# Kernel tuning notes

Hardware: AMD Instinct MI355X
Metric: run time of the kernel (lower is better)

## Reference

```python
import jax, jax.numpy as jnp
import numpy as np

B, S, D = 8, 4096, 1024


def setup_inputs() -> dict:
    key = jax.random.key(0)
    kq, kk, kv, kw, kb = jax.random.split(key, 5)
    query = jax.random.normal(kq, (B, S, D), dtype=jnp.float32)
    k = jax.random.normal(kk, (B, S, D), dtype=jnp.float32)
    value = jax.random.normal(kv, (B, S, D), dtype=jnp.float32)
    # nn.Linear(hidden_size, hidden_size) params (Kaiming-uniform-ish init scale)
    bound = 1.0 / np.sqrt(D)
    W_out = jax.random.uniform(kw, (D, D), minval=-bound, maxval=bound, dtype=jnp.float32)
    b_out = jax.random.uniform(kb, (D,), minval=-bound, maxval=bound, dtype=jnp.float32)
    return {"query": query, "key": k, "value": value, "W_out": W_out, "b_out": b_out}


def reference(query, key, value, W_out, b_out):
    d = query.shape[-1]
    scale = 1.0 / jnp.sqrt(jnp.asarray(d, dtype=query.dtype))
    # scores: [B, Sq, Sk]
    scores = jnp.einsum("bqd,bkd->bqk", query, key) * scale
    attn = jax.nn.softmax(scores, axis=-1)
    # training=False -> dropout is identity
    ctx = jnp.einsum("bqk,bkd->bqd", attn, value)
    # nn.Linear: x @ W^T + b
    out = jnp.einsum("bqd,ed->bqe", ctx, W_out) + b_out
    return out
```

## Files before the change

kernel.cpp:

```cpp
#include <hip/hip_runtime.h>
#include <hip/hip_bf16.h>

typedef __attribute__((ext_vector_type(4))) float f4;
typedef __attribute__((ext_vector_type(4))) short s4;
typedef __attribute__((ext_vector_type(8))) short s8;

#define SEQ 4096
#define DIM 1024
#define NB 8

__device__ inline short f2bf(float f) {
    return __builtin_bit_cast(short, __float2bfloat16(f));
}

__device__ inline float bf2f(short s) {
    return __builtin_bit_cast(float, (unsigned)((unsigned short)s) << 16);
}

__device__ inline void gload_lds16(const void* g, void* l) {
    __builtin_amdgcn_global_load_lds(
        (const __attribute__((address_space(1))) void*)g,
        (__attribute__((address_space(3))) void*)l, 16, 0, 0);
}

template<int OUT>
__global__ __launch_bounds__(512, 2) void gemm256(
    const short* __restrict__ A, size_t lda, size_t bsA,
    const short* __restrict__ B, size_t ldb, size_t bsB,
    void* __restrict__ C, size_t ldc, size_t bsC,
    const float* __restrict__ bias, int nt, int gridN)
{
    __shared__ short lds[2 * 32768];
    const int tid  = threadIdx.x;
    const int lane = tid & 63;
    const int wave = tid >> 6;

    A += (size_t)blockIdx.y * bsA;
    B += (size_t)blockIdx.y * bsB;
    float* Cf = (float*)C + (size_t)blockIdx.y * bsC;
    short* Cs = (short*)C + (size_t)blockIdx.y * bsC;

    const int nwg = gridDim.x;
    int wg = blockIdx.x;
    wg = (wg & 7) * (nwg >> 3) + (wg >> 3);
    const size_t tm = (size_t)(wg / gridN) * 256;
    const size_t tn = (size_t)(wg % gridN) * 256;

    const int srow = tid >> 3;
    const int slot = tid & 7;
    const int sc   = slot ^ (srow & 7);
    const short* pA = A + (tm + srow) * lda + sc * 8;
    const short* pB = B + (tn + srow) * ldb + sc * 8;
    const int ldst = srow * 64 + slot * 8;

    const int fr = lane & 15, kg = lane >> 4;
    const int wr = wave >> 2, wc = wave & 3;

    auto STAGE = [&](int t) {
        short* bufA = lds + (t & 1) * 32768;
        short* bufB = bufA + 16384;
        const size_t k0 = (size_t)t * 64;
        #pragma unroll
        for (int j = 0; j < 4; ++j) {
            gload_lds16(pA + (size_t)(j * 64) * lda + k0, bufA + j * 4096 + ldst);
            gload_lds16(pB + (size_t)(j * 64) * ldb + k0, bufB + j * 4096 + ldst);
        }
    };

    f4 acc[8][4];
    #pragma unroll
    for (int m = 0; m < 8; ++m)
        #pragma unroll
        for (int n = 0; n < 4; ++n)
            acc[m][n] = (f4){0.f, 0.f, 0.f, 0.f};

    STAGE(0);
    __syncthreads();

    for (int t = 0; t < nt; ++t) {
        if (t + 1 < nt) STAGE(t + 1);

        const short* bufA = lds + (t & 1) * 32768;
        const short* bufB = bufA + 16384;
        s8 af[2][8], bf[2][4];
        #pragma unroll
        for (int kh = 0; kh < 2; ++kh) {
            #pragma unroll
            for (int m = 0; m < 8; ++m) {
                const int row = wr * 128 + m * 16 + fr;
                const int c   = kh * 4 + kg;
                af[kh][m] = *(const s8*)(bufA + row * 64 + (c ^ (row & 7)) * 8);
            }
            #pragma unroll
            for (int n = 0; n < 4; ++n) {
                const int row = wc * 64 + n * 16 + fr;
                const int c   = kh * 4 + kg;
                bf[kh][n] = *(const s8*)(bufB + row * 64 + (c ^ (row & 7)) * 8);
            }
        }
        __builtin_amdgcn_s_setprio(1);
        #pragma unroll
        for (int kh = 0; kh < 2; ++kh)
            #pragma unroll
            for (int m = 0; m < 8; ++m)
                #pragma unroll
                for (int n = 0; n < 4; ++n)
                    acc[m][n] = __builtin_amdgcn_mfma_f32_16x16x32_bf16(
                        af[kh][m], bf[kh][n], acc[m][n], 0, 0, 0);
        __builtin_amdgcn_s_setprio(0);

        __syncthreads();
    }

    const int cg = lane >> 4, cl = lane & 15;
    #pragma unroll
    for (int m = 0; m < 8; ++m) {
        #pragma unroll
        for (int n = 0; n < 4; ++n) {
            const size_t grow = tm + wr * 128 + m * 16 + cg * 4;
            const size_t gcol = tn + wc * 64 + n * 16 + cl;
            float bv = 0.f;
            if constexpr (OUT == 0) { if (bias) bv = bias[gcol]; }
            #pragma unroll
            for (int i = 0; i < 4; ++i) {
                const float val = acc[m][n][i] + bv;
                if constexpr (OUT == 0)
                    Cf[(grow + i) * ldc + gcol] = val;
                else
                    Cs[(grow + i) * ldc + gcol] = f2bf(val);
            }
        }
    }
}

__global__ __launch_bounds__(256) void conv_bf16(const float* __restrict__ in,
                                                 short* __restrict__ out, int n8)
{
    const int i = blockIdx.x * 256 + threadIdx.x;
    if (i >= n8) return;
    f4 a = ((const f4*)in)[2 * i];
    f4 b = ((const f4*)in)[2 * i + 1];
    s8 w;
    w[0] = f2bf(a[0]); w[1] = f2bf(a[1]); w[2] = f2bf(a[2]); w[3] = f2bf(a[3]);
    w[4] = f2bf(b[0]); w[5] = f2bf(b[1]); w[6] = f2bf(b[2]); w[7] = f2bf(b[3]);
    ((s8*)out)[i] = w;
}

__global__ __launch_bounds__(256) void prep_batch(
    const float* __restrict__ Qf, const float* __restrict__ Kf,
    const float* __restrict__ Vf,
    short* __restrict__ Qb, short* __restrict__ Kb, short* __restrict__ VT)
{
    const int tid = threadIdx.x;
    const int blk = blockIdx.x;

    if (blk < 4096) {
        const float* in = (blk < 2048) ? Qf : Kf;
        short* out      = (blk < 2048) ? Qb : Kb;
        const int i = (blk & 2047) * 256 + tid;
        f4 a = ((const f4*)in)[2 * i];
        f4 b = ((const f4*)in)[2 * i + 1];
        s8 w;
        w[0] = f2bf(a[0]); w[1] = f2bf(a[1]); w[2] = f2bf(a[2]); w[3] = f2bf(a[3]);
        w[4] = f2bf(b[0]); w[5] = f2bf(b[1]); w[6] = f2bf(b[2]); w[7] = f2bf(b[3]);
        ((s8*)out)[i] = w;
    } else {
        __shared__ float t[32][33];
        const int b2 = blk - 4096;
        const size_t k0 = (size_t)(b2 & 127) * 32;
        const size_t d0 = (size_t)(b2 >> 7) * 32;

        const int r = tid >> 3, c4 = (tid & 7) * 4;
        f4 x = *(const f4*)(Vf + (k0 + r) * DIM + d0 + c4);
        #pragma unroll
        for (int i = 0; i < 4; ++i) t[r][c4 + i] = x[i];
        __syncthreads();

        const int d = tid >> 3, kk = (tid & 7) * 4;
        s4 w;
        #pragma unroll
        for (int i = 0; i < 4; ++i) w[i] = f2bf(t[kk + i][d]);
        *(s4*)(VT + (d0 + d) * SEQ + k0 + kk) = w;
    }
}

__global__ __launch_bounds__(256) void softmax_rows_bf(short* __restrict__ scores)
{
    const int tid = threadIdx.x;
    short* srow = scores + (size_t)blockIdx.y * SEQ * SEQ + (size_t)blockIdx.x * SEQ;
    const float SCALE = 0.03125f;

    float v[16];
    float mx = -3.4e38f;
    #pragma unroll
    for (int j = 0; j < 4; ++j) {
        s4 h = *(const s4*)(srow + (size_t)(j * 256 + tid) * 4);
        #pragma unroll
        for (int i = 0; i < 4; ++i) {
            const float f = bf2f(h[i]) * SCALE;
            v[j * 4 + i] = f;
            mx = fmaxf(mx, f);
        }
    }
    #pragma unroll
    for (int o = 32; o > 0; o >>= 1) mx = fmaxf(mx, __shfl_xor(mx, o));
    __shared__ float red[4];
    if ((tid & 63) == 0) red[tid >> 6] = mx;
    __syncthreads();
    mx = fmaxf(fmaxf(red[0], red[1]), fmaxf(red[2], red[3]));

    float sum = 0.f;
    #pragma unroll
    for (int j = 0; j < 16; ++j) {
        const float e = __expf(v[j] - mx);
        v[j] = e;
        sum += e;
    }
    #pragma unroll
    for (int o = 32; o > 0; o >>= 1) sum += __shfl_xor(sum, o);
    __syncthreads();
    if ((tid & 63) == 0) red[tid >> 6] = sum;
    __syncthreads();
    const float inv = 1.f / (red[0] + red[1] + red[2] + red[3]);

    #pragma unroll
    for (int j = 0; j < 4; ++j) {
        s4 w;
        #pragma unroll
        for (int i = 0; i < 4; ++i) w[i] = f2bf(v[j * 4 + i] * inv);
        *(s4*)(srow + (size_t)(j * 256 + tid) * 4) = w;
    }
}

extern "C" void kernel_launch(void* const* d_in, const int* in_sizes, int n_in,
                              void* d_out, int out_size, void* d_ws, size_t ws_size,
                              hipStream_t stream) {
    const float* Q    = (const float*)d_in[0];
    const float* Km   = (const float*)d_in[1];
    const float* V    = (const float*)d_in[2];
    const float* W    = (const float*)d_in[3];
    const float* bias = (const float*)d_in[4];
    float* out = (float*)d_out;

    short* ctx = (short*)d_ws;
    short* VT4 = ctx + (size_t)NB * SEQ * DIM;
    short* Qb  = VT4 + (size_t)4 * DIM * SEQ;
    short* Kb  = Qb + (size_t)SEQ * DIM;
    short* Wb  = Kb + (size_t)SEQ * DIM;
    short* scoresB = (short*)d_out;

    const dim3 blk256(256), blk512(512);
    conv_bf16<<<DIM * DIM / 2048, blk256, 0, stream>>>(W, Wb, DIM * DIM / 8);

    for (int g = 0; g < 2; ++g) {
        for (int b4 = 0; b4 < 4; ++b4) {
            const int b = g * 4 + b4;
            const float* Qf = Q  + (size_t)b * SEQ * DIM;
            const float* Kf = Km + (size_t)b * SEQ * DIM;
            const float* Vf = V  + (size_t)b * SEQ * DIM;

            prep_batch<<<dim3(8192), blk256, 0, stream>>>(
                Qf, Kf, Vf, Qb, Kb, VT4 + (size_t)b4 * DIM * SEQ);

            gemm256<2><<<dim3(256, 1), blk512, 0, stream>>>(
                Qb, DIM, 0, Kb, DIM, 0,
                scoresB + (size_t)b4 * SEQ * SEQ, SEQ, 0,
                nullptr, DIM / 64, 16);
        }
        softmax_rows_bf<<<dim3(SEQ, 4), blk256, 0, stream>>>(scoresB);

        gemm256<2><<<dim3(64, 4), blk512, 0, stream>>>(
            scoresB, SEQ, (size_t)SEQ * SEQ,
            VT4, SEQ, (size_t)DIM * SEQ,
            ctx + (size_t)g * 4 * SEQ * DIM, DIM, (size_t)SEQ * DIM,
            nullptr, SEQ / 64, 4);
    }

    gemm256<0><<<dim3(512, 1), blk512, 0, stream>>>(
        ctx, DIM, 0, Wb, DIM, 0, out, DIM, 0, bias, DIM / 64, 4);
}
```

Baseline: 811.8 us.

## Split GEMM LDS staging into half-tiles with explicit vmcnt-based prefetch pipeline

Restructures the 256x256 bf16 GEMM main loop so that LDS holds four half-tile buffers instead of two full-tile buffers. Loads for the next two half-tiles are issued right after the fragment reads finish, so they overlap with the MFMA block. Synchronisation moves from __syncthreads to explicit vmcnt/lgkmcnt waits plus raw s_barrier, which removes the full drain of outstanding loads each iteration. The risk is subtle: the hand-counted vmcnt thresholds and buffer reuse must match the number of loads in flight, or races appear.

```diff
diff --git a/kernel.cpp b/kernel.cpp
--- a/kernel.cpp
+++ b/kernel.cpp
@@ -30,7 +30,7 @@
     void* __restrict__ C, size_t ldc, size_t bsC,
     const float* __restrict__ bias, int nt, int gridN)
 {
-    __shared__ short lds[2 * 32768];
+    __shared__ short lds[4 * 16384];
     const int tid  = threadIdx.x;
     const int lane = tid & 63;
     const int wave = tid >> 6;
@@ -56,14 +56,14 @@
     const int fr = lane & 15, kg = lane >> 4;
     const int wr = wave >> 2, wc = wave & 3;
 
-    auto STAGE = [&](int t) {
-        short* bufA = lds + (t & 1) * 32768;
-        short* bufB = bufA + 16384;
-        const size_t k0 = (size_t)t * 64;
-        #pragma unroll
-        for (int j = 0; j < 4; ++j) {
-            gload_lds16(pA + (size_t)(j * 64) * lda + k0, bufA + j * 4096 + ldst);
-            gload_lds16(pB + (size_t)(j * 64) * ldb + k0, bufB + j * 4096 + ldst);
+    auto SH = [&](int h) {
+        short* hb = lds + (h & 3) * 16384;
+        const size_t k0 = (size_t)(h >> 1) * 64;
+        const size_t rb = (size_t)(h & 1) * 128;
+        #pragma unroll
+        for (int j = 0; j < 2; ++j) {
+            gload_lds16(pA + (rb + j * 64) * lda + k0, hb + j * 4096 + ldst);
+            gload_lds16(pB + (rb + j * 64) * ldb + k0, hb + 8192 + j * 4096 + ldst);
         }
     };
 
@@ -74,30 +74,38 @@
         for (int n = 0; n < 4; ++n)
             acc[m][n] = (f4){0.f, 0.f, 0.f, 0.f};
 
-    STAGE(0);
-    __syncthreads();
+    SH(0); SH(1); SH(2); SH(3);
+    asm volatile("s_waitcnt vmcnt(8)" ::: "memory");
+    __builtin_amdgcn_s_barrier();
+    __builtin_amdgcn_sched_barrier(0);
 
     for (int t = 0; t < nt; ++t) {
-        if (t + 1 < nt) STAGE(t + 1);
-
-        const short* bufA = lds + (t & 1) * 32768;
-        const short* bufB = bufA + 16384;
+        const short* hb0 = lds + ((2 * t) & 3) * 16384;
+        const short* hb1 = lds + ((2 * t + 1) & 3) * 16384;
+        const short* hA = wr ? hb1 : hb0;
+        const short* hB = ((wc >> 1) ? hb1 : hb0) + 8192;
+
         s8 af[2][8], bf[2][4];
         #pragma unroll
         for (int kh = 0; kh < 2; ++kh) {
             #pragma unroll
             for (int m = 0; m < 8; ++m) {
-                const int row = wr * 128 + m * 16 + fr;
-                const int c   = kh * 4 + kg;
-                af[kh][m] = *(const s8*)(bufA + row * 64 + (c ^ (row & 7)) * 8);
+                const int rh = m * 16 + fr;
+                af[kh][m] = *(const s8*)(hA + rh * 64 + ((kh * 4 + kg) ^ (rh & 7)) * 8);
             }
             #pragma unroll
             for (int n = 0; n < 4; ++n) {
-                const int row = wc * 64 + n * 16 + fr;
-                const int c   = kh * 4 + kg;
-                bf[kh][n] = *(const s8*)(bufB + row * 64 + (c ^ (row & 7)) * 8);
-            }
-        }
+                const int rh = (wc & 1) * 64 + n * 16 + fr;
+                bf[kh][n] = *(const s8*)(hB + rh * 64 + ((kh * 4 + kg) ^ (rh & 7)) * 8);
+            }
+        }
+        asm volatile("s_waitcnt lgkmcnt(0)" ::: "memory");
+        __builtin_amdgcn_sched_barrier(0);
+        __builtin_amdgcn_s_barrier();
+        __builtin_amdgcn_sched_barrier(0);
+
+        if (t + 2 < nt) { SH(2 * t + 4); SH(2 * t + 5); }
+
         __builtin_amdgcn_s_setprio(1);
         #pragma unroll
         for (int kh = 0; kh < 2; ++kh)
@@ -109,7 +117,15 @@
                         af[kh][m], bf[kh][n], acc[m][n], 0, 0, 0);
         __builtin_amdgcn_s_setprio(0);
 
-        __syncthreads();
+        if (t + 1 < nt) {
+            if (t + 2 < nt) {
+                asm volatile("s_waitcnt vmcnt(8)" ::: "memory");
+            } else {
+                asm volatile("s_waitcnt vmcnt(0)" ::: "memory");
+            }
+            __builtin_amdgcn_s_barrier();
+            __builtin_amdgcn_sched_barrier(0);
+        }
     }
 
     const int cg = lane >> 4, cl = lane & 15;
```

Result: slower. 829.6 us (+2.2%).

## Shrink GEMM tile to 128x256 with BK=32 for four blocks per CU

Applied to the files above, without the earlier changes.

Replaces the 256x256x64 GEMM tile with a 128x256x32 tile, new swizzled LDS staging, and launch bounds requesting four 512-thread blocks per CU. LDS use drops to 48KB and the accumulators to a 4x4 MFMA set, so more waves can be resident to hide latency, and grids double so there are more blocks to spread across CUs. In exchange each tile has lower arithmetic intensity (more global and LDS traffic per FLOP) and runs twice as many K iterations, each with a barrier.

```diff
diff --git a/kernel.cpp b/kernel.cpp
--- a/kernel.cpp
+++ b/kernel.cpp
@@ -24,13 +24,13 @@
 }
 
 template<int OUT>
-__global__ __launch_bounds__(512, 2) void gemm256(
+__global__ __launch_bounds__(512, 4) void gemmB(
     const short* __restrict__ A, size_t lda, size_t bsA,
     const short* __restrict__ B, size_t ldb, size_t bsB,
     void* __restrict__ C, size_t ldc, size_t bsC,
     const float* __restrict__ bias, int nt, int gridN)
 {
-    __shared__ short lds[2 * 32768];
+    __shared__ short lds[2 * 12288];
     const int tid  = threadIdx.x;
     const int lane = tid & 63;
     const int wave = tid >> 6;
@@ -43,33 +43,30 @@
     const int nwg = gridDim.x;
     int wg = blockIdx.x;
     wg = (wg & 7) * (nwg >> 3) + (wg >> 3);
-    const size_t tm = (size_t)(wg / gridN) * 256;
+    const size_t tm = (size_t)(wg / gridN) * 128;
     const size_t tn = (size_t)(wg % gridN) * 256;
 
-    const int srow = tid >> 3;
-    const int slot = tid & 7;
-    const int sc   = slot ^ (srow & 7);
+    const int srow = tid >> 2;
+    const int sc   = (tid & 3) ^ ((tid >> 3) & 3);
     const short* pA = A + (tm + srow) * lda + sc * 8;
     const short* pB = B + (tn + srow) * ldb + sc * 8;
-    const int ldst = srow * 64 + slot * 8;
+    const size_t b128 = (size_t)128 * ldb;
 
     const int fr = lane & 15, kg = lane >> 4;
+    const int ck = kg ^ ((fr >> 1) & 3);
     const int wr = wave >> 2, wc = wave & 3;
 
     auto STAGE = [&](int t) {
-        short* bufA = lds + (t & 1) * 32768;
-        short* bufB = bufA + 16384;
-        const size_t k0 = (size_t)t * 64;
-        #pragma unroll
-        for (int j = 0; j < 4; ++j) {
-            gload_lds16(pA + (size_t)(j * 64) * lda + k0, bufA + j * 4096 + ldst);
-            gload_lds16(pB + (size_t)(j * 64) * ldb + k0, bufB + j * 4096 + ldst);
-        }
+        short* buf = lds + (t & 1) * 12288;
+        const size_t k0 = (size_t)t * 32;
+        gload_lds16(pA + k0,        buf + tid * 8);
+        gload_lds16(pB + k0,        buf + 4096 + tid * 8);
+        gload_lds16(pB + b128 + k0, buf + 8192 + tid * 8);
     };
 
-    f4 acc[8][4];
-    #pragma unroll
-    for (int m = 0; m < 8; ++m)
+    f4 acc[4][4];
+    #pragma unroll
+    for (int m = 0; m < 4; ++m)
         #pragma unroll
         for (int n = 0; n < 4; ++n)
             acc[m][n] = (f4){0.f, 0.f, 0.f, 0.f};
@@ -80,33 +77,26 @@
     for (int t = 0; t < nt; ++t) {
         if (t + 1 < nt) STAGE(t + 1);
 
-        const short* bufA = lds + (t & 1) * 32768;
-        const short* bufB = bufA + 16384;
-        s8 af[2][8], bf[2][4];
-        #pragma unroll
-        for (int kh = 0; kh < 2; ++kh) {
+        const short* bufA = lds + (t & 1) * 12288;
+        const short* bufB = bufA + 4096;
+        s8 af[4], bf[4];
+        #pragma unroll
+        for (int m = 0; m < 4; ++m) {
+            const int row = wr * 64 + m * 16 + fr;
+            af[m] = *(const s8*)(bufA + row * 32 + ck * 8);
+        }
+        #pragma unroll
+        for (int n = 0; n < 4; ++n) {
+            const int row = wc * 64 + n * 16 + fr;
+            bf[n] = *(const s8*)(bufB + row * 32 + ck * 8);
+        }
+        __builtin_amdgcn_s_setprio(1);
+        #pragma unroll
+        for (int m = 0; m < 4; ++m)
             #pragma unroll
-            for (int m = 0; m < 8; ++m) {
-                const int row = wr * 128 + m * 16 + fr;
-                const int c   = kh * 4 + kg;
-                af[kh][m] = *(const s8*)(bufA + row * 64 + (c ^ (row & 7)) * 8);
-            }
-            #pragma unroll
-            for (int n = 0; n < 4; ++n) {
-                const int row = wc * 64 + n * 16 + fr;
-                const int c   = kh * 4 + kg;
-                bf[kh][n] = *(const s8*)(bufB + row * 64 + (c ^ (row & 7)) * 8);
-            }
-        }
-        __builtin_amdgcn_s_setprio(1);
-        #pragma unroll
-        for (int kh = 0; kh < 2; ++kh)
-            #pragma unroll
-            for (int m = 0; m < 8; ++m)
-                #pragma unroll
-                for (int n = 0; n < 4; ++n)
-                    acc[m][n] = __builtin_amdgcn_mfma_f32_16x16x32_bf16(
-                        af[kh][m], bf[kh][n], acc[m][n], 0, 0, 0);
+            for (int n = 0; n < 4; ++n)
+                acc[m][n] = __builtin_amdgcn_mfma_f32_16x16x32_bf16(
+                    af[m], bf[n], acc[m][n], 0, 0, 0);
         __builtin_amdgcn_s_setprio(0);
 
         __syncthreads();
@@ -114,10 +104,10 @@
 
     const int cg = lane >> 4, cl = lane & 15;
     #pragma unroll
-    for (int m = 0; m < 8; ++m) {
+    for (int m = 0; m < 4; ++m) {
         #pragma unroll
         for (int n = 0; n < 4; ++n) {
-            const size_t grow = tm + wr * 128 + m * 16 + cg * 4;
+            const size_t grow = tm + wr * 64 + m * 16 + cg * 4;
             const size_t gcol = tn + wc * 64 + n * 16 + cl;
             float bv = 0.f;
             if constexpr (OUT == 0) { if (bias) bv = bias[gcol]; }
@@ -262,20 +252,20 @@
             prep_batch<<<dim3(8192), blk256, 0, stream>>>(
                 Qf, Kf, Vf, Qb, Kb, VT4 + (size_t)b4 * DIM * SEQ);
 
-            gemm256<2><<<dim3(256, 1), blk512, 0, stream>>>(
+            gemmB<2><<<dim3(512, 1), blk512, 0, stream>>>(
                 Qb, DIM, 0, Kb, DIM, 0,
                 scoresB + (size_t)b4 * SEQ * SEQ, SEQ, 0,
-                nullptr, DIM / 64, 16);
+                nullptr, DIM / 32, 16);
         }
         softmax_rows_bf<<<dim3(SEQ, 4), blk256, 0, stream>>>(scoresB);
 
-        gemm256<2><<<dim3(64, 4), blk512, 0, stream>>>(
+        gemmB<2><<<dim3(128, 4), blk512, 0, stream>>>(
             scoresB, SEQ, (size_t)SEQ * SEQ,
             VT4, SEQ, (size_t)DIM * SEQ,
             ctx + (size_t)g * 4 * SEQ * DIM, DIM, (size_t)SEQ * DIM,
-            nullptr, SEQ / 64, 4);
-    }
-
-    gemm256<0><<<dim3(512, 1), blk512, 0, stream>>>(
-        ctx, DIM, 0, Wb, DIM, 0, out, DIM, 0, bias, DIM / 64, 4);
-}
+            nullptr, SEQ / 32, 4);
+    }
+
+    gemmB<0><<<dim3(1024, 1), blk512, 0, stream>>>(
+        ctx, DIM, 0, Wb, DIM, 0, out, DIM, 0, bias, DIM / 32, 4);
+}
```

New measurement: 872.3 us. +7.4%, slower.

## Split GEMM main loop into four phases interleaving LDS reads, prefetch, and MFMA

Applied to the files above, without the earlier changes.

Restructures the bf16 GEMM main loop into four sub-phases per K-tile. Each phase loads a slice of A fragments from LDS, issues one quarter of the next tile's global-to-LDS prefetch, and runs the matching MFMAs, with explicit barriers and waitcnts in place of one bulk load and a single __syncthreads. The aim is to overlap memory traffic with matrix work and cut register pressure from holding all A fragments at once. The extra per-phase barriers add synchronisation cost and could stall waves.

```diff
diff --git a/kernel.cpp b/kernel.cpp
--- a/kernel.cpp
+++ b/kernel.cpp
@@ -56,15 +56,12 @@
     const int fr = lane & 15, kg = lane >> 4;
     const int wr = wave >> 2, wc = wave & 3;
 
-    auto STAGE = [&](int t) {
+    auto STAGE2 = [&](int t, int p) {
         short* bufA = lds + (t & 1) * 32768;
         short* bufB = bufA + 16384;
         const size_t k0 = (size_t)t * 64;
-        #pragma unroll
-        for (int j = 0; j < 4; ++j) {
-            gload_lds16(pA + (size_t)(j * 64) * lda + k0, bufA + j * 4096 + ldst);
-            gload_lds16(pB + (size_t)(j * 64) * ldb + k0, bufB + j * 4096 + ldst);
-        }
+        gload_lds16(pA + (size_t)(p * 64) * lda + k0, bufA + p * 4096 + ldst);
+        gload_lds16(pB + (size_t)(p * 64) * ldb + k0, bufB + p * 4096 + ldst);
     };
 
     f4 acc[8][4];
@@ -74,42 +71,56 @@
         for (int n = 0; n < 4; ++n)
             acc[m][n] = (f4){0.f, 0.f, 0.f, 0.f};
 
-    STAGE(0);
+    STAGE2(0, 0); STAGE2(0, 1); STAGE2(0, 2); STAGE2(0, 3);
     __syncthreads();
 
     for (int t = 0; t < nt; ++t) {
-        if (t + 1 < nt) STAGE(t + 1);
-
         const short* bufA = lds + (t & 1) * 32768;
         const short* bufB = bufA + 16384;
-        s8 af[2][8], bf[2][4];
-        #pragma unroll
-        for (int kh = 0; kh < 2; ++kh) {
+        s8 bfrag[2][4];
+
+        #pragma unroll
+        for (int p = 0; p < 4; ++p) {
+            if (p == 0) {
+                #pragma unroll
+                for (int kh = 0; kh < 2; ++kh)
+                    #pragma unroll
+                    for (int n = 0; n < 4; ++n) {
+                        const int row = wc * 64 + n * 16 + fr;
+                        bfrag[kh][n] = *(const s8*)(bufB + row * 64 + (((kh * 4 + kg) ^ (row & 7)) * 8));
+                    }
+            }
+            s8 afrag[2][2];
             #pragma unroll
-            for (int m = 0; m < 8; ++m) {
-                const int row = wr * 128 + m * 16 + fr;
-                const int c   = kh * 4 + kg;
-                af[kh][m] = *(const s8*)(bufA + row * 64 + (c ^ (row & 7)) * 8);
-            }
+            for (int kh = 0; kh < 2; ++kh)
+                #pragma unroll
+                for (int m2 = 0; m2 < 2; ++m2) {
+                    const int row = wr * 128 + (2 * p + m2) * 16 + fr;
+                    afrag[kh][m2] = *(const s8*)(bufA + row * 64 + (((kh * 4 + kg) ^ (row & 7)) * 8));
+                }
+            if (t + 1 < nt) STAGE2(t + 1, p);
+
+            __builtin_amdgcn_s_barrier();
+            asm volatile("s_waitcnt lgkmcnt(0)" ::: "memory");
+            __builtin_amdgcn_sched_barrier(0);
+            __builtin_amdgcn_s_setprio(1);
             #pragma unroll
-            for (int n = 0; n < 4; ++n) {
-                const int row = wc * 64 + n * 16 + fr;
-                const int c   = kh * 4 + kg;
-                bf[kh][n] = *(const s8*)(bufB + row * 64 + (c ^ (row & 7)) * 8);
-            }
-        }
-        __builtin_amdgcn_s_setprio(1);
-        #pragma unroll
-        for (int kh = 0; kh < 2; ++kh)
-            #pragma unroll
-            for (int m = 0; m < 8; ++m)
+            for (int kh = 0; kh < 2; ++kh)
                 #pragma unroll
-                for (int n = 0; n < 4; ++n)
-                    acc[m][n] = __builtin_amdgcn_mfma_f32_16x16x32_bf16(
-                        af[kh][m], bf[kh][n], acc[m][n], 0, 0, 0);
-        __builtin_amdgcn_s_setprio(0);
-
-        __syncthreads();
+                for (int m2 = 0; m2 < 2; ++m2)
+                    #pragma unroll
+                    for (int n = 0; n < 4; ++n)
+                        acc[2 * p + m2][n] = __builtin_amdgcn_mfma_f32_16x16x32_bf16(
+                            afrag[kh][m2], bfrag[kh][n], acc[2 * p + m2][n], 0, 0, 0);
+            __builtin_amdgcn_s_setprio(0);
+            __builtin_amdgcn_s_barrier();
+        }
+
+        if (t + 1 < nt) {
+            asm volatile("s_waitcnt vmcnt(0)" ::: "memory");
+            __builtin_amdgcn_s_barrier();
+            __builtin_amdgcn_sched_barrier(0);
+        }
     }
 
     const int cg = lane >> 4, cl = lane & 15;
```

Measured after the change: 884.7 us. +9.0%, slower.
